# Performance work log

Hardware: AMD Instinct MI355X
Metric: run time of the kernel (lower is better)

Reference implementation:

```python
import jax, jax.numpy as jnp
import numpy as np

NUM_BINS = 5
KEEP_POLARITY = True
DT_OFFSET = 1


def setup_inputs() -> dict:
    key = jax.random.key(0)
    N = 10_000_000
    W, H = 1280, 720
    curr_time, delta_t = 100000, 50000
    k0, k1, k2, k3 = jax.random.split(key, 4)
    t0 = float(curr_time - delta_t)
    # timestamps sorted, strictly within the window (t <= curr_time)
    t = jnp.sort(jax.random.uniform(k0, (N,), minval=t0, maxval=float(curr_time)))
    x = jax.random.randint(k1, (N,), 0, W).astype(jnp.float32)
    y = jax.random.randint(k2, (N,), 0, H).astype(jnp.float32)
    p = (jax.random.randint(k3, (N,), 0, 2) * 2 - 1).astype(jnp.float32)  # {-1,+1}
    events = jnp.stack([t, x, y, p], axis=1)  # [N,4]
    return {"events": events, "curr_time": curr_time, "delta_t": delta_t,
            "width": W, "height": H}


def reference(events, curr_time, delta_t, width, height):
    t = events[:, 0]
    x = events[:, 1]
    y = events[:, 2]
    p = events[:, 3]

    bt = float(curr_time - delta_t)          # window start t0
    dt = float(delta_t + DT_OFFSET)          # duration + offset

    # bilinear temporal weights
    bin_f = (NUM_BINS - 1.0) * (t - bt) / dt
    back = jnp.floor(bin_f)                  # t >= bt so trunc == floor
    fwd_w = bin_f - back
    back_i = back.astype(jnp.int32)
    fwd_i = back_i + 1

    bins = jnp.concatenate([back_i, fwd_i])              # [2N]
    kw = jnp.concatenate([1.0 - fwd_w, fwd_w])           # [2N]

    pos = (p > 0).astype(jnp.int32)
    pdim = 2 if KEEP_POLARITY else 1
    pos2 = jnp.concatenate([pos, pos])
    xi = jnp.concatenate([x, x]).astype(jnp.int32)
    yi = jnp.concatenate([y, y]).astype(jnp.int32)

    # measurement == 'time': value = weight * normalized timestamp
    tn = (t - bt) / dt
    vals = kw * jnp.concatenate([tn, tn])

    # flattened 4D index: [bin, polarity, y, x]
    flat = ((bins * pdim + pos2) * height + yi) * width + xi
    grid = jnp.zeros(NUM_BINS * pdim * height * width, jnp.float32)
    grid = grid.at[flat].add(vals)
    return grid.reshape(NUM_BINS * pdim, height, width)  # [C,H,W]
```

## Files before the change

### kernel.cpp

```cpp
#include <hip/hip_runtime.h>
#include <hip/hip_bf16.h>


#define NUM_BINS 5
#define DT_OFFSET 1
#define GW 1280
#define GH 720
#define NSLAB (NUM_BINS * 2)
#define NGRP 240
#define NB2 256
#define ITERS 40
#define GWP (GW + 4)
#define CURSOR_BYTES 4096
#define OF_RESERVE (512*1024)
#define MIN_CAPG 45056
#define FXS 8192.0f


__global__ __launch_bounds__(1024, 4) void p2_bucket(
        const float4* __restrict__ ev, int n,
        unsigned* __restrict__ cursor, unsigned* __restrict__ bucket,
        unsigned* __restrict__ oflist, int ofcap, int capg,
        const int* __restrict__ ct_p, const int* __restrict__ dt_p) {
    __shared__ unsigned hist[NGRP];
    __shared__ unsigned base[NGRP];

    const int chunk = (n + gridDim.x - 1) / gridDim.x;
    const int start = blockIdx.x * chunk;
    const int end   = min(n, start + chunk);

    if (threadIdx.x < NGRP) hist[threadIdx.x] = 0u;
    __syncthreads();

    const int ct  = *ct_p;
    const int dti = *dt_p;
    const float bt  = (float)(ct - dti);
    const float dtf = (float)(dti + DT_OFFSET);

    unsigned wk[ITERS];
    int      gj[ITERS];
    #pragma unroll
    for (int k = 0; k < ITERS; ++k) {
        int i = start + (int)threadIdx.x + k * 1024;
        gj[k] = -1;
        wk[k] = 0u;
        if (i < end) {
            float4 e = ev[i];
            int yi  = (int)e.z;
            int xi  = (int)e.y;
            int pos = (e.w > 0.0f) ? 1 : 0;
            int g   = yi / 3;
            int ylo = yi - 3 * g;
            float tn = (e.x - bt) / dtf;
            unsigned q = (unsigned)(tn * 65535.0f + 0.5f);
            if (q > 65535u) q = 65535u;
            wk[k] = (q << 14) | ((unsigned)ylo << 12)
                  | ((unsigned)pos << 11) | (unsigned)xi;
            unsigned j = atomicAdd(&hist[g], 1u);
            gj[k] = (int)((j << 8) | (unsigned)g);
        }
    }
    __syncthreads();

    if (threadIdx.x < NGRP) {
        unsigned k = threadIdx.x;
        unsigned c = hist[k];
        if (c) {
            unsigned r = (c + 15u) & ~15u;
            unsigned b = atomicAdd(&cursor[k], r);
            base[k] = b;
            unsigned* bk = bucket + (size_t)k * capg;
            for (unsigned j = c; j < r; ++j) {
                unsigned slot = b + j;
                if (slot < (unsigned)capg) bk[slot] = 0u;
            }
        } else {
            base[k] = 0u;
        }
    }
    __syncthreads();

    #pragma unroll
    for (int k = 0; k < ITERS; ++k) {
        if (gj[k] >= 0) {
            int      g = gj[k] & 255;
            unsigned j = (unsigned)gj[k] >> 8;
            unsigned slot = base[g] + j;
            if (slot < (unsigned)capg) {
                bucket[(size_t)g * capg + slot] = wk[k];
            } else {
                unsigned o = atomicAdd(&cursor[NGRP], 1u);
                if (o < (unsigned)ofcap) {
                    oflist[2 * o]     = (unsigned)(3 * g + ((wk[k] >> 12) & 3u));
                    oflist[2 * o + 1] = wk[k];
                }
            }
        }
    }
}

__device__ __forceinline__ void p3_process(unsigned w, unsigned mypos,
                                           unsigned* tile) {
    if (w == 0u) return;
    if (((w >> 11) & 1u) != mypos) return;
    int   xi  = (int)(w & 0x7FFu);
    int   ylo = (int)((w >> 12) & 3u);
    float qf  = (float)(w >> 14);
    float tn  = qf * (1.0f / 65535.0f);
    float bf  = qf * (4.0f / 65535.0f);
    float back = floorf(bf);
    float fw   = bf - back;
    int   b    = (int)back;
    if (b > NUM_BINS - 2) b = NUM_BINS - 2;
    unsigned ql = (unsigned)((1.0f - fw) * tn * FXS + 0.5f);
    unsigned qh = (unsigned)(fw * tn * FXS + 0.5f);
    int   k   = ((b & 1) << 1) | (b >> 1);
    int   idx = (ylo * GWP + xi) * 4 + k;
    atomicAdd(&tile[idx], ql | (qh << 16));
}

__global__ __launch_bounds__(1024) void p3_accum(
        const unsigned* __restrict__ cursor, const unsigned* __restrict__ bucket,
        float* __restrict__ out, int capg) {
    __shared__ unsigned tile[3 * GWP * 4];
    const int      g     = blockIdx.x % NGRP;
    const unsigned mypos = (unsigned)(blockIdx.x / NGRP);

    for (int k = threadIdx.x; k < 3 * GWP * 4; k += blockDim.x)
        tile[k] = 0u;
    __syncthreads();

    unsigned cnt = cursor[g];
    if (cnt > (unsigned)capg) cnt = (unsigned)capg;
    const uint4* bk4 = (const uint4*)(bucket + (size_t)g * capg);
    unsigned n4 = cnt / 4;

    const uint4 z4 = make_uint4(0u, 0u, 0u, 0u);
    for (unsigned j0 = threadIdx.x; j0 < n4; j0 += 4u * 1024u) {
        unsigned j1 = j0 + 1024u, j2 = j0 + 2048u, j3 = j0 + 3072u;
        uint4 a = bk4[j0];
        uint4 b = (j1 < n4) ? bk4[j1] : z4;
        uint4 c = (j2 < n4) ? bk4[j2] : z4;
        uint4 d = (j3 < n4) ? bk4[j3] : z4;
        p3_process(a.x, mypos, tile); p3_process(a.y, mypos, tile);
        p3_process(a.z, mypos, tile); p3_process(a.w, mypos, tile);
        p3_process(b.x, mypos, tile); p3_process(b.y, mypos, tile);
        p3_process(b.z, mypos, tile); p3_process(b.w, mypos, tile);
        p3_process(c.x, mypos, tile); p3_process(c.y, mypos, tile);
        p3_process(c.z, mypos, tile); p3_process(c.w, mypos, tile);
        p3_process(d.x, mypos, tile); p3_process(d.y, mypos, tile);
        p3_process(d.z, mypos, tile); p3_process(d.w, mypos, tile);
    }
    __syncthreads();

    for (int k = threadIdx.x; k < NUM_BINS * 3 * (GW / 4); k += blockDim.x) {
        int r   = k / (GW / 4);
        int x4  = k % (GW / 4);
        int b   = r / 3;
        int ylo = r - 3 * b;
        int y   = 3 * g + ylo;
        float4 o;
        float* po = (float*)&o;
        #pragma unroll
        for (int j = 0; j < 4; ++j) {
            int cidx = ylo * GWP + (x4 * 4 + j);
            uint4 wv = *(const uint4*)&tile[cidx * 4];
            unsigned v;
            if      (b == 0) v = (wv.x & 0xFFFFu);
            else if (b == 1) v = (wv.x >> 16) + (wv.z & 0xFFFFu);
            else if (b == 2) v = (wv.y & 0xFFFFu) + (wv.z >> 16);
            else if (b == 3) v = (wv.y >> 16) + (wv.w & 0xFFFFu);
            else             v = (wv.w >> 16);
            po[j] = (float)v * (1.0f / FXS);
        }
        ((float4*)(out + ((size_t)(b * 2 + (int)mypos) * GH + y) * GW))[x4] = o;
    }
}

__global__ void p4_overflow(const unsigned* __restrict__ cursor,
                            const unsigned* __restrict__ oflist, int ofcap,
                            float* __restrict__ out) {
    unsigned nof = cursor[NGRP];
    if (nof > (unsigned)ofcap) nof = (unsigned)ofcap;
    for (unsigned k = blockIdx.x * blockDim.x + threadIdx.x; k < nof;
         k += gridDim.x * blockDim.x) {
        unsigned yi = oflist[2 * k];
        unsigned w  = oflist[2 * k + 1];
        int   xi  = (int)(w & 0x7FFu);
        int   pos = (int)((w >> 11) & 1u);
        float tn  = (float)(w >> 14) * (1.0f / 65535.0f);
        float bf  = (NUM_BINS - 1.0f) * tn;
        float back = floorf(bf);
        float fw   = bf - back;
        int   b    = (int)back;
        if (b > NUM_BINS - 2) b = NUM_BINS - 2;
        atomicAdd(&out[((size_t)(b * 2 + pos) * GH + yi) * GW + xi],
                  (1.0f - fw) * tn);
        atomicAdd(&out[((size_t)((b + 1) * 2 + pos) * GH + yi) * GW + xi],
                  fw * tn);
    }
}

__global__ void voxel_scatter_kernel(const float4* __restrict__ events,
                                     float* __restrict__ out, int n,
                                     const int* __restrict__ ct_p,
                                     const int* __restrict__ dt_p,
                                     const int* __restrict__ w_p,
                                     const int* __restrict__ h_p) {
    int i = blockIdx.x * blockDim.x + threadIdx.x;
    if (i >= n) return;
    const int ct = *ct_p, dti = *dt_p, W = *w_p, H = *h_p;
    const float bt  = (float)(ct - dti);
    const float dtf = (float)(dti + DT_OFFSET);
    float4 e = events[i];
    const float tn    = (e.x - bt) / dtf;
    const float bin_f = (NUM_BINS - 1.0f) * tn;
    const float back  = floorf(bin_f);
    const float fwd_w = bin_f - back;
    const int back_i = (int)back;
    const int pos    = (e.w > 0.0f) ? 1 : 0;
    const int xi = (int)e.y, yi = (int)e.z;
    const int plane = H * W, slab = 2 * plane;
    const int base = (back_i * 2 + pos) * plane + yi * W + xi;
    atomicAdd(&out[base],        (1.0f - fwd_w) * tn);
    atomicAdd(&out[base + slab], fwd_w * tn);
}

extern "C" void kernel_launch(void* const* d_in, const int* in_sizes, int n_in,
                              void* d_out, int out_size, void* d_ws, size_t ws_size,
                              hipStream_t stream) {
    const float4* events = (const float4*)d_in[0];
    const int* curr_time = (const int*)d_in[1];
    const int* delta_t   = (const int*)d_in[2];
    const int* width     = (const int*)d_in[3];
    const int* height    = (const int*)d_in[4];
    float* out = (float*)d_out;
    const int n = in_sizes[0] / 4;

    int capg = 0;
    if (ws_size > CURSOR_BYTES + OF_RESERVE)
        capg = (int)(((ws_size - CURSOR_BYTES - OF_RESERVE)
                      / (NGRP * sizeof(unsigned))) & ~(size_t)15);

    if (capg >= MIN_CAPG && n <= NB2 * 1024 * ITERS) {
        unsigned* cursor = (unsigned*)d_ws;
        unsigned* bucket = (unsigned*)((char*)d_ws + CURSOR_BYTES);
        unsigned* oflist = bucket + (size_t)NGRP * capg;
        int ofcap = (int)((ws_size - CURSOR_BYTES
                           - (size_t)NGRP * capg * sizeof(unsigned))
                          / (2 * sizeof(unsigned)));
        hipMemsetAsync(cursor, 0, CURSOR_BYTES, stream);
        p2_bucket<<<NB2, 1024, 0, stream>>>(events, n, cursor, bucket,
                                            oflist, ofcap, capg,
                                            curr_time, delta_t);
        p3_accum<<<2 * NGRP, 1024, 0, stream>>>(cursor, bucket, out, capg);
        p4_overflow<<<64, 256, 0, stream>>>(cursor, oflist, ofcap, out);
    } else {
        hipMemsetAsync(out, 0, (size_t)out_size * sizeof(float), stream);
        const int block = 256;
        const int grid  = (n + block - 1) / block;
        voxel_scatter_kernel<<<grid, block, 0, stream>>>(events, n ? out : out, n,
                                                         curr_time, delta_t,
                                                         width, height);
    }
}
```

Before: 312.6 us.

## Chunk bucketing pass with prefetched event loads and unpadded bucket reservations

Restructures the bucketing kernel to handle its 40 events per thread in 5 chunks of 8. Each chunk gets its own shared histogram and global cursor reservation, and the next chunk's events are loaded while the current chunk is scattered. This cuts register pressure (the occupancy hint is dropped) and overlaps loads with the scatter, at the cost of more block barriers and more global cursor atomics. Reservations are no longer padded to 16 with zero fill, so the accumulate kernel gains a scalar tail loop for counts not divisible by 4.

```diff
diff --git a/kernel.cpp b/kernel.cpp
--- a/kernel.cpp
+++ b/kernel.cpp
@@ -9,7 +9,9 @@
 #define NSLAB (NUM_BINS * 2)
 #define NGRP 240
 #define NB2 256
-#define ITERS 40
+#define CH 5
+#define EPT 8
+#define ITERS (CH * EPT)
 #define GWP (GW + 4)
 #define CURSOR_BYTES 4096
 #define OF_RESERVE (512*1024)
@@ -17,7 +19,7 @@
 #define FXS 8192.0f
 
 
-__global__ __launch_bounds__(1024, 4) void p2_bucket(
+__global__ __launch_bounds__(1024) void p2_bucket(
         const float4* __restrict__ ev, int n,
         unsigned* __restrict__ cursor, unsigned* __restrict__ bucket,
         unsigned* __restrict__ oflist, int ofcap, int capg,
@@ -28,8 +30,9 @@
     const int chunk = (n + gridDim.x - 1) / gridDim.x;
     const int start = blockIdx.x * chunk;
     const int end   = min(n, start + chunk);
-
-    if (threadIdx.x < NGRP) hist[threadIdx.x] = 0u;
+    const int tid   = (int)threadIdx.x;
+
+    if (tid < NGRP) hist[tid] = 0u;
     __syncthreads();
 
     const int ct  = *ct_p;
@@ -37,62 +40,67 @@
     const float bt  = (float)(ct - dti);
     const float dtf = (float)(dti + DT_OFFSET);
 
-    unsigned wk[ITERS];
-    int      gj[ITERS];
+    float4 e[EPT];
     #pragma unroll
-    for (int k = 0; k < ITERS; ++k) {
-        int i = start + (int)threadIdx.x + k * 1024;
-        gj[k] = -1;
-        wk[k] = 0u;
-        if (i < end) {
-            float4 e = ev[i];
-            int yi  = (int)e.z;
-            int xi  = (int)e.y;
-            int pos = (e.w > 0.0f) ? 1 : 0;
-            int g   = yi / 3;
-            int ylo = yi - 3 * g;
-            float tn = (e.x - bt) / dtf;
-            unsigned q = (unsigned)(tn * 65535.0f + 0.5f);
-            if (q > 65535u) q = 65535u;
-            wk[k] = (q << 14) | ((unsigned)ylo << 12)
-                  | ((unsigned)pos << 11) | (unsigned)xi;
-            unsigned j = atomicAdd(&hist[g], 1u);
-            gj[k] = (int)((j << 8) | (unsigned)g);
-        }
-    }
-    __syncthreads();
-
-    if (threadIdx.x < NGRP) {
-        unsigned k = threadIdx.x;
-        unsigned c = hist[k];
-        if (c) {
-            unsigned r = (c + 15u) & ~15u;
-            unsigned b = atomicAdd(&cursor[k], r);
-            base[k] = b;
-            unsigned* bk = bucket + (size_t)k * capg;
-            for (unsigned j = c; j < r; ++j) {
-                unsigned slot = b + j;
-                if (slot < (unsigned)capg) bk[slot] = 0u;
+    for (int k = 0; k < EPT; ++k) {
+        int i = start + tid + k * 1024;
+        if (i < end) e[k] = ev[i];
+    }
+
+    for (int c = 0; c < CH; ++c) {
+        unsigned wk[EPT];
+        int      gj[EPT];
+        #pragma unroll
+        for (int k = 0; k < EPT; ++k) {
+            int i = start + tid + (c * EPT + k) * 1024;
+            gj[k] = -1;
+            if (i < end) {
+                float4 ee = e[k];
+                int yi  = (int)ee.z;
+                int xi  = (int)ee.y;
+                int pos = (ee.w > 0.0f) ? 1 : 0;
+                int g   = yi / 3;
+                int ylo = yi - 3 * g;
+                float tn = (ee.x - bt) / dtf;
+                unsigned q = (unsigned)(tn * 65535.0f + 0.5f);
+                if (q > 65535u) q = 65535u;
+                wk[k] = (q << 14) | ((unsigned)ylo << 12)
+                      | ((unsigned)pos << 11) | (unsigned)xi;
+                unsigned j = atomicAdd(&hist[g], 1u);
+                gj[k] = (int)((j << 8) | (unsigned)g);
             }
-        } else {
-            base[k] = 0u;
-        }
-    }
-    __syncthreads();
-
-    #pragma unroll
-    for (int k = 0; k < ITERS; ++k) {
-        if (gj[k] >= 0) {
-            int      g = gj[k] & 255;
-            unsigned j = (unsigned)gj[k] >> 8;
-            unsigned slot = base[g] + j;
-            if (slot < (unsigned)capg) {
-                bucket[(size_t)g * capg + slot] = wk[k];
-            } else {
-                unsigned o = atomicAdd(&cursor[NGRP], 1u);
-                if (o < (unsigned)ofcap) {
-                    oflist[2 * o]     = (unsigned)(3 * g + ((wk[k] >> 12) & 3u));
-                    oflist[2 * o + 1] = wk[k];
+        }
+        __syncthreads();
+
+        if (tid < NGRP) {
+            unsigned cc = hist[tid];
+            if (cc) base[tid] = atomicAdd(&cursor[tid], cc);
+            hist[tid] = 0u;
+        }
+        __syncthreads();
+
+        if (c + 1 < CH) {
+            #pragma unroll
+            for (int k = 0; k < EPT; ++k) {
+                int i = start + tid + ((c + 1) * EPT + k) * 1024;
+                if (i < end) e[k] = ev[i];
+            }
+        }
+
+        #pragma unroll
+        for (int k = 0; k < EPT; ++k) {
+            if (gj[k] >= 0) {
+                int      g = gj[k] & 255;
+                unsigned j = (unsigned)gj[k] >> 8;
+                unsigned slot = base[g] + j;
+                if (slot < (unsigned)capg) {
+                    bucket[(size_t)g * capg + slot] = wk[k];
+                } else {
+                    unsigned o = atomicAdd(&cursor[NGRP], 1u);
+                    if (o < (unsigned)ofcap) {
+                        oflist[2 * o]     = (unsigned)(3 * g + ((wk[k] >> 12) & 3u));
+                        oflist[2 * o + 1] = wk[k];
+                    }
                 }
             }
         }
@@ -132,7 +140,8 @@
 
     unsigned cnt = cursor[g];
     if (cnt > (unsigned)capg) cnt = (unsigned)capg;
-    const uint4* bk4 = (const uint4*)(bucket + (size_t)g * capg);
+    const unsigned* bk = bucket + (size_t)g * capg;
+    const uint4* bk4 = (const uint4*)bk;
     unsigned n4 = cnt / 4;
 
     const uint4 z4 = make_uint4(0u, 0u, 0u, 0u);
@@ -151,6 +160,8 @@
         p3_process(d.x, mypos, tile); p3_process(d.y, mypos, tile);
         p3_process(d.z, mypos, tile); p3_process(d.w, mypos, tile);
     }
+    for (unsigned j = n4 * 4 + threadIdx.x; j < cnt; j += 1024)
+        p3_process(bk[j], mypos, tile);
     __syncthreads();
 
     for (int k = threadIdx.x; k < NUM_BINS * 3 * (GW / 4); k += blockDim.x) {
@@ -259,7 +270,7 @@
         hipMemsetAsync(out, 0, (size_t)out_size * sizeof(float), stream);
         const int block = 256;
         const int grid  = (n + block - 1) / block;
-        voxel_scatter_kernel<<<grid, block, 0, stream>>>(events, n ? out : out, n,
+        voxel_scatter_kernel<<<grid, block, 0, stream>>>(events, out, n,
                                                          curr_time, delta_t,
                                                          width, height);
     }
```

Result: no change. 309.2 us (-1.1%).
